# Performance work log

Hardware: AMD Instinct MI355X
Metric: run time of the kernel (lower is better)

## Reference

```python
import jax, jax.numpy as jnp
import numpy as np

B, S, H = 16, 1024, 256
NH = 4
DH = H // NH


def setup_inputs() -> dict:
    key = jax.random.key(0)
    ks = jax.random.split(key, 12)
    w = lambda i, shape: jax.random.normal(ks[i], shape, dtype=jnp.float32) * 0.02
    return {
        "step_sequence": jax.random.normal(ks[0], (B, S, H), dtype=jnp.float32),
        "final_outcomes": jax.random.normal(ks[1], (B,), dtype=jnp.float32),
        "step_mask": jnp.ones((B, S), dtype=jnp.bool_),
        # MultiheadAttention q/k projections (only attn weights are used)
        "Wq": w(2, (H, H)), "bq": jnp.zeros((H,), jnp.float32),
        "Wk": w(3, (H, H)), "bk": jnp.zeros((H,), jnp.float32),
        # causal_mask_predictor: Linear(H,H//2)-ReLU-Linear(H//2,1)-Sigmoid
        "Wm1": w(4, (H, H // 2)), "bm1": jnp.zeros((H // 2,), jnp.float32),
        "Wm2": w(5, (H // 2, 1)), "bm2": jnp.zeros((1,), jnp.float32),
        # intervention_generator: Linear(H,H)-ReLU-Linear(H,H)-Tanh
        "Wi1": w(6, (H, H)), "bi1": jnp.zeros((H,), jnp.float32),
        "Wi2": w(7, (H, H)), "bi2": jnp.zeros((H,), jnp.float32),
        # credit_estimator: Linear(H,H//2)-ReLU-Linear(H//2,1)
        "We1": w(8, (H, H // 2)), "be1": jnp.zeros((H // 2,), jnp.float32),
        "We2": w(9, (H // 2, 1)), "be2": jnp.zeros((1,), jnp.float32),
    }


def _forward(x, final_outcomes, step_mask, Wq, bq, Wk, bk, Wm1, bm1, Wm2, bm2,
             Wi1, bi1, Wi2, bi2, We1, be1, We2, be2):
    # --- CausalAttentionModule ---
    q = (x @ Wq + bq).reshape(B, S, NH, DH).transpose(0, 2, 1, 3)  # [B,NH,S,DH]
    k = (x @ Wk + bk).reshape(B, S, NH, DH).transpose(0, 2, 1, 3)
    scores = jnp.einsum('bhqd,bhkd->bhqk', q, k) / jnp.sqrt(jnp.float32(DH))
    scores = jnp.where(step_mask[:, None, None, :], scores, -jnp.inf)  # key_padding_mask
    attn = jax.nn.softmax(scores, axis=-1).mean(axis=1)  # head-averaged [B,S,S]
    strengths = jax.nn.sigmoid(jax.nn.relu(x @ Wm1 + bm1) @ Wm2 + bm2)[..., 0]  # [B,S]
    aw_mean = attn.mean(axis=1)  # mean over query dim -> [B,S]
    cm = aw_mean[:, None, :] * strengths[:, :, None]  # [B,S,S]
    cm = cm * jnp.tril(jnp.ones((S, S), dtype=x.dtype))[None]
    # --- interventional credit (vectorized over the B x S python loop) ---
    colmean = cm.mean(axis=1)  # mean_i cm[b,i,j] -> [B,S]
    base = (x * colmean[..., None]).mean(axis=1)  # [B,H] baseline weighted-mean feature
    # intervention changes only row t: delta = 0.1*tanh-MLP(x_t)
    delta = 0.1 * jnp.tanh(jax.nn.relu(x @ Wi1 + bi1) @ Wi2 + bi2)  # [B,S,H]
    feats = base[:, None, :] + delta * colmean[..., None] / S  # [B,S,H]
    outcomes = (jax.nn.relu(feats @ We1 + be1) @ We2 + be2)[..., 0]  # [B,S]
    credit = jnp.where(step_mask, final_outcomes[:, None] - outcomes, 0.0)
    return credit, cm


def reference(step_sequence, final_outcomes, step_mask, Wq, bq, Wk, bk,
              Wm1, bm1, Wm2, bm2, Wi1, bi1, Wi2, bi2, We1, be1, We2, be2):
    return _forward(step_sequence, final_outcomes, step_mask, Wq, bq, Wk, bk,
                    Wm1, bm1, Wm2, bm2, Wi1, bi1, Wi2, bi2, We1, be1, We2, be2)
```

## Files before the change

kernel.cpp:

```cpp
#include <hip/hip_runtime.h>
#include <hip/hip_bf16.h>
#include <math.h>

#define B 16
#define S 1024
#define H 256
#define NH 4
#define DH 64
#define BS (B*S)
#define XSTR 264
#define L2E 1.4426950408889634f

typedef short short8 __attribute__((ext_vector_type(8)));
typedef float f32x16 __attribute__((ext_vector_type(16)));

__device__ __forceinline__ unsigned short to_bf16(float v) {
  __hip_bfloat16 h = __float2bfloat16(v);
  return *(unsigned short*)&h;
}
__device__ __forceinline__ unsigned int pack_bf16x2(float a, float b) {
  return (unsigned int)to_bf16(a) | ((unsigned int)to_bf16(b) << 16);
}
__device__ __forceinline__ float exp2_hw(float v) {
  return __builtin_amdgcn_exp2f(v);
}
__device__ __forceinline__ float log2_hw(float v) {
  return __builtin_amdgcn_logf(v);
}

__global__ __launch_bounds__(256) void k_convert_w(
    const float* __restrict__ Wq, const float* __restrict__ Wk,
    const float* __restrict__ Wm1, const float* __restrict__ Wi1,
    const float* __restrict__ Wi2, const float* __restrict__ We1,
    unsigned short* __restrict__ WqT, unsigned short* __restrict__ WkT,
    unsigned short* __restrict__ Wm1T, unsigned short* __restrict__ Wi1T,
    unsigned short* __restrict__ Wi2T, unsigned short* __restrict__ We1T)
{
  const float* src; unsigned short* dst; int N;
  switch (blockIdx.y) {
    case 0: src = Wq;  dst = WqT;  N = 256; break;
    case 1: src = Wk;  dst = WkT;  N = 256; break;
    case 2: src = Wm1; dst = Wm1T; N = 128; break;
    case 3: src = Wi1; dst = Wi1T; N = 256; break;
    case 4: src = Wi2; dst = Wi2T; N = 256; break;
    default: src = We1; dst = We1T; N = 128; break;
  }
  int ntiles = N >> 5;
  int tile = blockIdx.x;
  if (tile >= 8 * ntiles) return;
  int kt = tile / ntiles, nt = tile % ntiles;
  __shared__ float tl[32][33];
  int t = threadIdx.x, r = t >> 5, c = t & 31;
  #pragma unroll
  for (int i = 0; i < 4; ++i)
    tl[r + i*8][c] = src[(kt*32 + r + i*8)*N + nt*32 + c];
  __syncthreads();
  #pragma unroll
  for (int i = 0; i < 4; ++i)
    dst[(nt*32 + r + i*8)*256 + kt*32 + c] = to_bf16(tl[c][r + i*8]);
}

__global__ __launch_bounds__(256) void k_qkproj_mfma(
    const float* __restrict__ x,
    const unsigned short* __restrict__ WqT, const unsigned short* __restrict__ WkT,
    const float* __restrict__ bq, const float* __restrict__ bk,
    unsigned short* __restrict__ qbuf, unsigned short* __restrict__ kbuf)
{
  __shared__ unsigned short xs[32*XSTR];
  int t = threadIdx.x, wave = t >> 6, lane = t & 63;
  int l5 = lane & 31, h5 = lane >> 5;
  int r0 = blockIdx.x * 32;
  {
    const float4* xg = (const float4*)(x + (size_t)r0*H);
    #pragma unroll
    for (int it = 0; it < 8; ++it) {
      int u = it*256 + t, r = u >> 6, c4 = u & 63;
      float4 v = xg[u];
      uint2 pk; pk.x = pack_bf16x2(v.x, v.y); pk.y = pack_bf16x2(v.z, v.w);
      *(uint2*)&xs[r*XSTR + c4*4] = pk;
    }
  }
  __syncthreads();
  int n0 = wave*64 + l5;
  f32x16 aq0, aq1, ak0, ak1;
  #pragma unroll
  for (int r = 0; r < 16; ++r) { aq0[r]=0.f; aq1[r]=0.f; ak0[r]=0.f; ak1[r]=0.f; }
  #pragma unroll 8
  for (int kc = 0; kc < 16; ++kc) {
    short8 a  = *(const short8*)&xs[l5*XSTR + kc*16 + h5*8];
    short8 q0 = *(const short8*)&WqT[(size_t)n0*256 + kc*16 + h5*8];
    short8 q1 = *(const short8*)&WqT[(size_t)(n0+32)*256 + kc*16 + h5*8];
    short8 k0 = *(const short8*)&WkT[(size_t)n0*256 + kc*16 + h5*8];
    short8 k1 = *(const short8*)&WkT[(size_t)(n0+32)*256 + kc*16 + h5*8];
    aq0 = __builtin_amdgcn_mfma_f32_32x32x16_bf16(a, q0, aq0, 0, 0, 0);
    aq1 = __builtin_amdgcn_mfma_f32_32x32x16_bf16(a, q1, aq1, 0, 0, 0);
    ak0 = __builtin_amdgcn_mfma_f32_32x32x16_bf16(a, k0, ak0, 0, 0, 0);
    ak1 = __builtin_amdgcn_mfma_f32_32x32x16_bf16(a, k1, ak1, 0, 0, 0);
  }
  const float qsc = 0.125f * L2E;
  __syncthreads();
  {
    float b0 = bq[n0], b1 = bq[n0+32];
    #pragma unroll
    for (int r = 0; r < 16; ++r) {
      int row = (r & 3) + 8*(r >> 2) + 4*h5;
      xs[row*XSTR + n0]      = to_bf16((aq0[r] + b0) * qsc);
      xs[row*XSTR + n0 + 32] = to_bf16((aq1[r] + b1) * qsc);
    }
  }
  __syncthreads();
  #pragma unroll
  for (int it = 0; it < 4; ++it) {
    int u = it*256 + t, r = u >> 5, c8 = u & 31;
    int mg = r0 + r, bb = mg >> 10, s = mg & 1023;
    int hh = c8 >> 3, dd = (c8 & 7) * 8;
    *(uint4*)&qbuf[(size_t)(((bb*NH + hh)*S + s)*DH + dd)] = *(uint4*)&xs[r*XSTR + c8*8];
  }
  __syncthreads();
  {
    float b0 = bk[n0], b1 = bk[n0+32];
    #pragma unroll
    for (int r = 0; r < 16; ++r) {
      int row = (r & 3) + 8*(r >> 2) + 4*h5;
      xs[row*XSTR + n0]      = to_bf16(ak0[r] + b0);
      xs[row*XSTR + n0 + 32] = to_bf16(ak1[r] + b1);
    }
  }
  __syncthreads();
  #pragma unroll
  for (int it = 0; it < 4; ++it) {
    int u = it*256 + t, r = u >> 5, c8 = u & 31;
    int mg = r0 + r, bb = mg >> 10, s = mg & 1023;
    int hh = c8 >> 3, dd = (c8 & 7) * 8;
    *(uint4*)&kbuf[(size_t)(((bb*NH + hh)*S + s)*DH + dd)] = *(uint4*)&xs[r*XSTR + c8*8];
  }
}

__global__ __launch_bounds__(256) void k_strengths_mfma(
    const float* __restrict__ x, const unsigned short* __restrict__ Wm1T,
    const float* __restrict__ bm1, const float* __restrict__ Wm2, const float* __restrict__ bm2,
    float* __restrict__ strengths)
{
  __shared__ unsigned short xs[32*XSTR];
  __shared__ float red[4][32];
  int t = threadIdx.x, wave = t >> 6, lane = t & 63;
  int l5 = lane & 31, h5 = lane >> 5;
  int r0 = blockIdx.x * 32;
  {
    const float4* xg = (const float4*)(x + (size_t)r0*H);
    #pragma unroll
    for (int it = 0; it < 8; ++it) {
      int u = it*256 + t, r = u >> 6, c4 = u & 63;
      float4 v = xg[u];
      uint2 pk; pk.x = pack_bf16x2(v.x, v.y); pk.y = pack_bf16x2(v.z, v.w);
      *(uint2*)&xs[r*XSTR + c4*4] = pk;
    }
  }
  __syncthreads();
  f32x16 acc;
  #pragma unroll
  for (int r = 0; r < 16; ++r) acc[r] = 0.f;
  int n = wave*32 + l5;
  #pragma unroll 8
  for (int kc = 0; kc < 16; ++kc) {
    short8 a = *(const short8*)&xs[l5*XSTR + kc*16 + h5*8];
    short8 b = *(const short8*)&Wm1T[(size_t)n*256 + kc*16 + h5*8];
    acc = __builtin_amdgcn_mfma_f32_32x32x16_bf16(a, b, acc, 0, 0, 0);
  }
  float bi = bm1[n], w2 = Wm2[n];
  #pragma unroll
  for (int r = 0; r < 16; ++r) {
    float v = fmaxf(acc[r] + bi, 0.f) * w2;
    #pragma unroll
    for (int off = 1; off <= 16; off <<= 1) v += __shfl_xor(v, off);
    if (l5 == 0) red[wave][(r & 3) + 8*(r >> 2) + 4*h5] = v;
  }
  __syncthreads();
  if (t < 32) {
    float s = red[0][t] + red[1][t] + red[2][t] + red[3][t] + bm2[0];
    strengths[r0 + t] = 1.f / (1.f + __expf(-s));
  }
}

__global__ __launch_bounds__(256) void k_attn_mfma(
    const unsigned short* __restrict__ qbuf, const unsigned short* __restrict__ kbuf,
    float* __restrict__ aw_part)
{
  __shared__ float part[4][32];
  int t = threadIdx.x, wave = t >> 6, lane = t & 63;
  int l5 = lane & 31, h5 = lane >> 5;
  int qt = blockIdx.x, i0 = qt * 32;
  int h = blockIdx.y, b = blockIdx.z;
  const unsigned short* qg = qbuf + (size_t)((b*NH + h)*S + i0) * DH;
  const unsigned short* kg = kbuf + (size_t)((b*NH + h)*S) * DH;

  short8 af[4];
  #pragma unroll
  for (int kc = 0; kc < 4; ++kc)
    af[kc] = *(const short8*)(qg + l5*DH + kc*16 + h5*8);

  float lacc[16];
  #pragma unroll
  for (int r = 0; r < 16; ++r) lacc[r] = 0.f;

  for (int kt = 0; kt < 8; ++kt) {
    short8 bfr[4];
    #pragma unroll
    for (int kc = 0; kc < 4; ++kc)
      bfr[kc] = *(const short8*)(kg + (size_t)(kt*128 + wave*32 + l5)*DH + kc*16 + h5*8);
    f32x16 acc;
    #pragma unroll
    for (int r = 0; r < 16; ++r) acc[r] = 0.f;
    #pragma unroll
    for (int kc = 0; kc < 4; ++kc)
      acc = __builtin_amdgcn_mfma_f32_32x32x16_bf16(af[kc], bfr[kc], acc, 0, 0, 0);
    #pragma unroll
    for (int r = 0; r < 16; ++r) lacc[r] += exp2_hw(acc[r]);
  }
  #pragma unroll
  for (int r = 0; r < 16; ++r) {
    float v = lacc[r];
    #pragma unroll
    for (int off = 1; off <= 16; off <<= 1) v += __shfl_xor(v, off);
    lacc[r] = v;
  }
  if (l5 == 0) {
    #pragma unroll
    for (int r = 0; r < 16; ++r)
      part[wave][(r & 3) + 8*(r >> 2) + 4*h5] = lacc[r];
  }
  __syncthreads();
  float llog[16];
  #pragma unroll
  for (int r = 0; r < 16; ++r) {
    int row = (r & 3) + 8*(r >> 2) + 4*h5;
    llog[r] = log2_hw(part[0][row] + part[1][row] + part[2][row] + part[3][row]);
  }
  for (int kt = 0; kt < 8; ++kt) {
    short8 bfr[4];
    #pragma unroll
    for (int kc = 0; kc < 4; ++kc)
      bfr[kc] = *(const short8*)(kg + (size_t)(kt*128 + wave*32 + l5)*DH + kc*16 + h5*8);
    f32x16 acc;
    #pragma unroll
    for (int r = 0; r < 16; ++r) acc[r] = 0.f;
    #pragma unroll
    for (int kc = 0; kc < 4; ++kc)
      acc = __builtin_amdgcn_mfma_f32_32x32x16_bf16(af[kc], bfr[kc], acc, 0, 0, 0);
    float csum = 0.f;
    #pragma unroll
    for (int r = 0; r < 16; ++r) csum += exp2_hw(acc[r] - llog[r]);
    csum += __shfl_xor(csum, 32);
    if (lane < 32)
      aw_part[(size_t)qt*BS + b*S + kt*128 + wave*32 + l5] = csum;
  }
}

__global__ __launch_bounds__(256) void k_colmean(
    const float* __restrict__ strengths, const float* __restrict__ aw_part,
    float* __restrict__ aw_mean, float* __restrict__ colmean)
{
  __shared__ float st[1024];
  int t = threadIdx.x, b = blockIdx.x;
  #pragma unroll
  for (int e = 0; e < 4; ++e) st[t + e*256] = strengths[b*S + t + e*256];
  __syncthreads();
  for (int off = 1; off < 1024; off <<= 1) {
    float tmp[4];
    #pragma unroll
    for (int e = 0; e < 4; ++e) {
      int j = t + e*256;
      tmp[e] = (j + off < 1024) ? st[j + off] : 0.f;
    }
    __syncthreads();
    #pragma unroll
    for (int e = 0; e < 4; ++e) st[t + e*256] += tmp[e];
    __syncthreads();
  }
  #pragma unroll
  for (int e = 0; e < 4; ++e) {
    int j = t + e*256;
    float s = 0.f;
    #pragma unroll
    for (int qt = 0; qt < 32; ++qt) s += aw_part[(size_t)qt*BS + b*S + j];
    float am = s * (1.f / (NH * (float)S));
    aw_mean[b*S + j] = am;
    colmean[b*S + j] = am * st[j] * (1.f / (float)S);
  }
}

__global__ __launch_bounds__(256) void k_cm(
    const float* __restrict__ aw_mean, const float* __restrict__ strengths,
    float* __restrict__ cm_out)
{
  int t = threadIdx.x;
  int row = blockIdx.x;
  int b = row >> 10, i = row & 1023;
  float sti = strengths[row];
  float4 v = ((const float4*)(aw_mean + b*S))[t];
  int j0 = t * 4;
  float4 o;
  o.x = (j0 + 0 <= i) ? v.x * sti : 0.f;
  o.y = (j0 + 1 <= i) ? v.y * sti : 0.f;
  o.z = (j0 + 2 <= i) ? v.z * sti : 0.f;
  o.w = (j0 + 3 <= i) ? v.w * sti : 0.f;
  ((float4*)cm_out)[(size_t)row*(S/4) + t] = o;
}

__global__ __launch_bounds__(256) void k_base(
    const float* __restrict__ x, const float* __restrict__ colmean,
    float* __restrict__ base_part)
{
  int t = threadIdx.x;
  int chunk = blockIdx.x, b = blockIdx.y;
  float acc = 0.f;
  int t0 = chunk * 32;
  for (int tt = 0; tt < 32; ++tt) {
    int srow = t0 + tt;
    acc += x[(size_t)(b*S + srow)*H + t] * colmean[b*S + srow];
  }
  base_part[(size_t)chunk*B*H + b*H + t] = acc * (1.f / (float)S);
}

__global__ __launch_bounds__(256) void k_credit_mfma(
    const float* __restrict__ x, const float* __restrict__ base_part,
    const float* __restrict__ colmean,
    const unsigned short* __restrict__ Wi1T, const float* __restrict__ bi1,
    const unsigned short* __restrict__ Wi2T, const float* __restrict__ bi2,
    const unsigned short* __restrict__ We1T, const float* __restrict__ be1,
    const float* __restrict__ We2, const float* __restrict__ be2,
    const float* __restrict__ final_outcomes, float* __restrict__ credit_out)
{
  __shared__ unsigned short xs[32*XSTR];
  __shared__ unsigned short hs[32*XSTR];
  __shared__ float cmv_s[32];
  __shared__ float red[4][32];
  int t = threadIdx.x, wave = t >> 6, lane = t & 63;
  int l5 = lane & 31, h5 = lane >> 5;
  int r0 = blockIdx.x * 32;
  int b = r0 >> 10;
  {
    const float4* xg = (const float4*)(x + (size_t)r0*H);
    #pragma unroll
    for (int it = 0; it < 8; ++it) {
      int u = it*256 + t, r = u >> 6, c4 = u & 63;
      float4 v = xg[u];
      uint2 pk; pk.x = pack_bf16x2(v.x, v.y); pk.y = pack_bf16x2(v.z, v.w);
      *(uint2*)&xs[r*XSTR + c4*4] = pk;
    }
  }
  if (t < 32) cmv_s[t] = colmean[r0 + t];
  int n0 = wave*64 + l5;
  float bb0 = 0.f, bb1 = 0.f;
  #pragma unroll
  for (int c = 0; c < 32; ++c) {
    bb0 += base_part[(size_t)c*B*H + b*H + n0];
    bb1 += base_part[(size_t)c*B*H + b*H + n0 + 32];
  }
  __syncthreads();

  {
    f32x16 acc0, acc1;
    #pragma unroll
    for (int r = 0; r < 16; ++r) { acc0[r] = 0.f; acc1[r] = 0.f; }
    #pragma unroll 8
    for (int kc = 0; kc < 16; ++kc) {
      short8 a = *(const short8*)&xs[l5*XSTR + kc*16 + h5*8];
      short8 b0 = *(const short8*)&Wi1T[(size_t)n0*256 + kc*16 + h5*8];
      short8 b1 = *(const short8*)&Wi1T[(size_t)(n0+32)*256 + kc*16 + h5*8];
      acc0 = __builtin_amdgcn_mfma_f32_32x32x16_bf16(a, b0, acc0, 0, 0, 0);
      acc1 = __builtin_amdgcn_mfma_f32_32x32x16_bf16(a, b1, acc1, 0, 0, 0);
    }
    float bi0 = bi1[n0], biv1 = bi1[n0 + 32];
    #pragma unroll
    for (int r = 0; r < 16; ++r) {
      int row = (r & 3) + 8*(r >> 2) + 4*h5;
      hs[row*XSTR + n0]      = to_bf16(fmaxf(acc0[r] + bi0, 0.f));
      hs[row*XSTR + n0 + 32] = to_bf16(fmaxf(acc1[r] + biv1, 0.f));
    }
  }
  __syncthreads();
  {
    f32x16 acc0, acc1;
    #pragma unroll
    for (int r = 0; r < 16; ++r) { acc0[r] = 0.f; acc1[r] = 0.f; }
    #pragma unroll 8
    for (int kc = 0; kc < 16; ++kc) {
      short8 a = *(const short8*)&hs[l5*XSTR + kc*16 + h5*8];
      short8 b0 = *(const short8*)&Wi2T[(size_t)n0*256 + kc*16 + h5*8];
      short8 b1 = *(const short8*)&Wi2T[(size_t)(n0+32)*256 + kc*16 + h5*8];
      acc0 = __builtin_amdgcn_mfma_f32_32x32x16_bf16(a, b0, acc0, 0, 0, 0);
      acc1 = __builtin_amdgcn_mfma_f32_32x32x16_bf16(a, b1, acc1, 0, 0, 0);
    }
    float bi0 = bi2[n0], biv1 = bi2[n0 + 32];
    __syncthreads();
    #pragma unroll
    for (int r = 0; r < 16; ++r) {
      int row = (r & 3) + 8*(r >> 2) + 4*h5;
      float cmv = cmv_s[row] * (0.1f / (float)S);
      float e0 = __expf(2.f*(acc0[r] + bi0));
      float e1 = __expf(2.f*(acc1[r] + biv1));
      float th0 = (e0 - 1.f) / (e0 + 1.f);
      float th1 = (e1 - 1.f) / (e1 + 1.f);
      xs[row*XSTR + n0]      = to_bf16(bb0 + th0 * cmv);
      xs[row*XSTR + n0 + 32] = to_bf16(bb1 + th1 * cmv);
    }
  }
  __syncthreads();
  {
    f32x16 acc;
    #pragma unroll
    for (int r = 0; r < 16; ++r) acc[r] = 0.f;
    int n = wave*32 + l5;
    #pragma unroll 8
    for (int kc = 0; kc < 16; ++kc) {
      short8 a = *(const short8*)&xs[l5*XSTR + kc*16 + h5*8];
      short8 bfrag = *(const short8*)&We1T[(size_t)n*256 + kc*16 + h5*8];
      acc = __builtin_amdgcn_mfma_f32_32x32x16_bf16(a, bfrag, acc, 0, 0, 0);
    }
    float bev = be1[n], w2 = We2[n];
    #pragma unroll
    for (int r = 0; r < 16; ++r) {
      float v = fmaxf(acc[r] + bev, 0.f) * w2;
      #pragma unroll
      for (int off = 1; off <= 16; off <<= 1) v += __shfl_xor(v, off);
      if (l5 == 0) red[wave][(r & 3) + 8*(r >> 2) + 4*h5] = v;
    }
  }
  __syncthreads();
  if (t < 32) {
    float s = red[0][t] + red[1][t] + red[2][t] + red[3][t] + be2[0];
    credit_out[r0 + t] = final_outcomes[b] - s;
  }
}

extern "C" void kernel_launch(void* const* d_in, const int* in_sizes, int n_in,
                              void* d_out, int out_size, void* d_ws, size_t ws_size,
                              hipStream_t stream) {
  (void)in_sizes; (void)n_in; (void)out_size; (void)ws_size;
  const float* x   = (const float*)d_in[0];
  const float* fin = (const float*)d_in[1];
  const float* Wq  = (const float*)d_in[3];  const float* bq  = (const float*)d_in[4];
  const float* Wk  = (const float*)d_in[5];  const float* bk  = (const float*)d_in[6];
  const float* Wm1 = (const float*)d_in[7];  const float* bm1 = (const float*)d_in[8];
  const float* Wm2 = (const float*)d_in[9];  const float* bm2 = (const float*)d_in[10];
  const float* Wi1 = (const float*)d_in[11]; const float* bi1 = (const float*)d_in[12];
  const float* Wi2 = (const float*)d_in[13]; const float* bi2 = (const float*)d_in[14];
  const float* We1 = (const float*)d_in[15]; const float* be1 = (const float*)d_in[16];
  const float* We2 = (const float*)d_in[17]; const float* be2 = (const float*)d_in[18];

  unsigned short* us = (unsigned short*)d_ws;
  unsigned short* qb   = us;
  unsigned short* kb   = qb + (size_t)B*NH*S*DH;
  unsigned short* WqT  = kb + (size_t)B*NH*S*DH;
  unsigned short* WkT  = WqT + 65536;
  unsigned short* Wi1T = WkT + 65536;
  unsigned short* Wi2T = Wi1T + 65536;
  unsigned short* Wm1T = Wi2T + 65536;
  unsigned short* We1T = Wm1T + 32768;
  float* fs = (float*)(We1T + 32768);
  float* aw_part   = fs;
  float* strengths = aw_part + 32*BS;
  float* aw_mean   = strengths + BS;
  float* colmean   = aw_mean + BS;
  float* base_part = colmean + BS;

  float* credit_out = (float*)d_out;
  float* cm_out     = credit_out + BS;

  k_convert_w     <<<dim3(64, 6), 256, 0, stream>>>(Wq, Wk, Wm1, Wi1, Wi2, We1,
                                                    WqT, WkT, Wm1T, Wi1T, Wi2T, We1T);
  k_qkproj_mfma   <<<BS/32, 256, 0, stream>>>(x, WqT, WkT, bq, bk, qb, kb);
  k_strengths_mfma<<<BS/32, 256, 0, stream>>>(x, Wm1T, bm1, Wm2, bm2, strengths);
  k_attn_mfma     <<<dim3(S/32, NH, B), 256, 0, stream>>>(qb, kb, aw_part);
  k_colmean       <<<B, 256, 0, stream>>>(strengths, aw_part, aw_mean, colmean);
  k_base          <<<dim3(32, B), 256, 0, stream>>>(x, colmean, base_part);
  k_cm            <<<BS, 256, 0, stream>>>(aw_mean, strengths, cm_out);
  k_credit_mfma   <<<BS/32, 256, 0, stream>>>(x, base_part, colmean, Wi1T, bi1, Wi2T, bi2,
                                              We1T, be1, We2, be2, fin, credit_out);
}
```

Baseline: 250.1 us.

## Stage K tiles in LDS and give each wave its own query rows in attention

```diff
diff --git a/kernel.cpp b/kernel.cpp
--- a/kernel.cpp
+++ b/kernel.cpp
@@ -182,16 +182,18 @@
   }
 }
 
+#define KSTR 68
 __global__ __launch_bounds__(256) void k_attn_mfma(
     const unsigned short* __restrict__ qbuf, const unsigned short* __restrict__ kbuf,
     float* __restrict__ aw_part)
 {
-  __shared__ float part[4][32];
+  __shared__ unsigned short Ks[256*KSTR];
+  __shared__ float colpart[4][1024];
   int t = threadIdx.x, wave = t >> 6, lane = t & 63;
   int l5 = lane & 31, h5 = lane >> 5;
-  int qt = blockIdx.x, i0 = qt * 32;
+  int qc = blockIdx.x;
   int h = blockIdx.y, b = blockIdx.z;
-  const unsigned short* qg = qbuf + (size_t)((b*NH + h)*S + i0) * DH;
+  const unsigned short* qg = qbuf + (size_t)((b*NH + h)*S + qc*128 + wave*32) * DH;
   const unsigned short* kg = kbuf + (size_t)((b*NH + h)*S) * DH;
 
   short8 af[4];
@@ -203,56 +205,72 @@
   #pragma unroll
   for (int r = 0; r < 16; ++r) lacc[r] = 0.f;
 
-  for (int kt = 0; kt < 8; ++kt) {
-    short8 bfr[4];
-    #pragma unroll
-    for (int kc = 0; kc < 4; ++kc)
-      bfr[kc] = *(const short8*)(kg + (size_t)(kt*128 + wave*32 + l5)*DH + kc*16 + h5*8);
-    f32x16 acc;
-    #pragma unroll
-    for (int r = 0; r < 16; ++r) acc[r] = 0.f;
-    #pragma unroll
-    for (int kc = 0; kc < 4; ++kc)
-      acc = __builtin_amdgcn_mfma_f32_32x32x16_bf16(af[kc], bfr[kc], acc, 0, 0, 0);
-    #pragma unroll
-    for (int r = 0; r < 16; ++r) lacc[r] += exp2_hw(acc[r]);
+  for (int c = 0; c < 4; ++c) {
+    __syncthreads();
+    const uint4* src = (const uint4*)(kg + (size_t)c*256*DH);
+    #pragma unroll
+    for (int it = 0; it < 8; ++it) {
+      int u = it*256 + t, key = u >> 3, c8 = u & 7;
+      *(uint4*)&Ks[key*KSTR + c8*8] = src[u];
+    }
+    __syncthreads();
+    #pragma unroll
+    for (int kt = 0; kt < 8; ++kt) {
+      short8 bfr[4];
+      #pragma unroll
+      for (int kc = 0; kc < 4; ++kc)
+        bfr[kc] = *(const short8*)&Ks[(kt*32 + l5)*KSTR + kc*16 + h5*8];
+      f32x16 acc;
+      #pragma unroll
+      for (int r = 0; r < 16; ++r) acc[r] = 0.f;
+      #pragma unroll
+      for (int kc = 0; kc < 4; ++kc)
+        acc = __builtin_amdgcn_mfma_f32_32x32x16_bf16(af[kc], bfr[kc], acc, 0, 0, 0);
+      #pragma unroll
+      for (int r = 0; r < 16; ++r) lacc[r] += exp2_hw(acc[r]);
+    }
   }
   #pragma unroll
   for (int r = 0; r < 16; ++r) {
     float v = lacc[r];
     #pragma unroll
     for (int off = 1; off <= 16; off <<= 1) v += __shfl_xor(v, off);
-    lacc[r] = v;
-  }
-  if (l5 == 0) {
-    #pragma unroll
-    for (int r = 0; r < 16; ++r)
-      part[wave][(r & 3) + 8*(r >> 2) + 4*h5] = lacc[r];
-  }
-  __syncthreads();
-  float llog[16];
-  #pragma unroll
-  for (int r = 0; r < 16; ++r) {
-    int row = (r & 3) + 8*(r >> 2) + 4*h5;
-    llog[r] = log2_hw(part[0][row] + part[1][row] + part[2][row] + part[3][row]);
-  }
-  for (int kt = 0; kt < 8; ++kt) {
-    short8 bfr[4];
-    #pragma unroll
-    for (int kc = 0; kc < 4; ++kc)
-      bfr[kc] = *(const short8*)(kg + (size_t)(kt*128 + wave*32 + l5)*DH + kc*16 + h5*8);
-    f32x16 acc;
-    #pragma unroll
-    for (int r = 0; r < 16; ++r) acc[r] = 0.f;
-    #pragma unroll
-    for (int kc = 0; kc < 4; ++kc)
-      acc = __builtin_amdgcn_mfma_f32_32x32x16_bf16(af[kc], bfr[kc], acc, 0, 0, 0);
-    float csum = 0.f;
-    #pragma unroll
-    for (int r = 0; r < 16; ++r) csum += exp2_hw(acc[r] - llog[r]);
-    csum += __shfl_xor(csum, 32);
-    if (lane < 32)
-      aw_part[(size_t)qt*BS + b*S + kt*128 + wave*32 + l5] = csum;
+    lacc[r] = log2_hw(v);
+  }
+  for (int c = 0; c < 4; ++c) {
+    __syncthreads();
+    const uint4* src = (const uint4*)(kg + (size_t)c*256*DH);
+    #pragma unroll
+    for (int it = 0; it < 8; ++it) {
+      int u = it*256 + t, key = u >> 3, c8 = u & 7;
+      *(uint4*)&Ks[key*KSTR + c8*8] = src[u];
+    }
+    __syncthreads();
+    #pragma unroll
+    for (int kt = 0; kt < 8; ++kt) {
+      short8 bfr[4];
+      #pragma unroll
+      for (int kc = 0; kc < 4; ++kc)
+        bfr[kc] = *(const short8*)&Ks[(kt*32 + l5)*KSTR + kc*16 + h5*8];
+      f32x16 acc;
+      #pragma unroll
+      for (int r = 0; r < 16; ++r) acc[r] = -lacc[r];
+      #pragma unroll
+      for (int kc = 0; kc < 4; ++kc)
+        acc = __builtin_amdgcn_mfma_f32_32x32x16_bf16(af[kc], bfr[kc], acc, 0, 0, 0);
+      float csum = 0.f;
+      #pragma unroll
+      for (int r = 0; r < 16; ++r) csum += exp2_hw(acc[r]);
+      csum += __shfl_xor(csum, 32);
+      if (h5 == 0) colpart[wave][c*256 + kt*32 + l5] = csum;
+    }
+  }
+  __syncthreads();
+  #pragma unroll
+  for (int e = 0; e < 4; ++e) {
+    int j = e*256 + t;
+    float s = colpart[0][j] + colpart[1][j] + colpart[2][j] + colpart[3][j];
+    aw_part[(size_t)qc*BS + b*S + j] = s;
   }
 }
 
@@ -282,7 +300,7 @@
     int j = t + e*256;
     float s = 0.f;
     #pragma unroll
-    for (int qt = 0; qt < 32; ++qt) s += aw_part[(size_t)qt*BS + b*S + j];
+    for (int qt = 0; qt < 8; ++qt) s += aw_part[(size_t)qt*BS + b*S + j];
     float am = s * (1.f / (NH * (float)S));
     aw_mean[b*S + j] = am;
     colmean[b*S + j] = am * st[j] * (1.f / (float)S);
@@ -460,7 +478,7 @@
   unsigned short* We1T = Wm1T + 32768;
   float* fs = (float*)(We1T + 32768);
   float* aw_part   = fs;
-  float* strengths = aw_part + 32*BS;
+  float* strengths = aw_part + 8*BS;
   float* aw_mean   = strengths + BS;
   float* colmean   = aw_mean + BS;
   float* base_part = colmean + BS;
@@ -472,7 +490,7 @@
                                                     WqT, WkT, Wm1T, Wi1T, Wi2T, We1T);
   k_qkproj_mfma   <<<BS/32, 256, 0, stream>>>(x, WqT, WkT, bq, bk, qb, kb);
   k_strengths_mfma<<<BS/32, 256, 0, stream>>>(x, Wm1T, bm1, Wm2, bm2, strengths);
-  k_attn_mfma     <<<dim3(S/32, NH, B), 256, 0, stream>>>(qb, kb, aw_part);
+  k_attn_mfma     <<<dim3(S/128, NH, B), 256, 0, stream>>>(qb, kb, aw_part);
   k_colmean       <<<B, 256, 0, stream>>>(strengths, aw_part, aw_mean, colmean);
   k_base          <<<dim3(32, B), 256, 0, stream>>>(x, colmean, base_part);
   k_cm            <<<BS, 256, 0, stream>>>(aw_mean, strengths, cm_out);
```

Result: faster. 221.7 us (-11.3%).
